# Optimization experiments

Hardware: AMD Instinct MI355X
Metric: run time of the kernel (lower is better)

The kernel has to match this reference:

```python
import jax, jax.numpy as jnp
import numpy as np

SEQ, LABEL, PRED = 96, 48, 96
DEC_LEN = LABEL + PRED  # 144
D_MODEL, N_HEADS, D_FF, C, NF = 512, 8, 2048, 7, 4
E = D_MODEL // N_HEADS  # 64
M_ENC = min(64, SEQ // 2)      # 48 modes, encoder self-attn
M_DEC = min(64, DEC_LEN // 2)  # 64 modes, decoder self / cross-q
M_KV = min(64, SEQ // 2)       # 48 modes, cross-kv
KMA = 25                       # moving-average kernel
E_LAYERS = 2
B = 128


def series_decomp(x):
    # moving average with edge replication padding (matches torch AvgPool1d version)
    p = (KMA - 1) // 2
    xp = jnp.concatenate([jnp.repeat(x[:, :1], p, axis=1), x, jnp.repeat(x[:, -1:], p, axis=1)], axis=1)
    cs = jnp.cumsum(xp, axis=1)
    cs = jnp.concatenate([jnp.zeros_like(cs[:, :1]), cs], axis=1)
    mean = (cs[:, KMA:] - cs[:, :-KMA]) / KMA  # [B,L,C]
    return x - mean, mean


def circ_conv(x, w):
    # Conv1d kernel=3, padding=1, padding_mode='circular', no bias. x [B,L,Cin], w [Cout,Cin,3]
    xp = jnp.concatenate([x[:, -1:], x, x[:, :1]], axis=1)
    return (jnp.einsum('blc,oc->blo', xp[:, :-2], w[:, :, 0])
            + jnp.einsum('blc,oc->blo', xp[:, 1:-1], w[:, :, 1])
            + jnp.einsum('blc,oc->blo', xp[:, 2:], w[:, :, 2]))


def my_layernorm(x, w, b):
    mu = jnp.mean(x, axis=-1, keepdims=True)
    var = jnp.mean((x - mu) ** 2, axis=-1, keepdims=True)
    xh = (x - mu) / jnp.sqrt(var + 1e-5) * w + b
    return xh - jnp.mean(xh, axis=1, keepdims=True)  # subtract per-batch time mean


def embed(x, mark, conv_w, time_w):
    # DataEmbedding_wo_pos: circular token conv + timeF linear (both bias-free)
    return circ_conv(x, conv_w) + mark @ time_w.T


def cplx(w):
    return jax.lax.complex(w[..., 0], w[..., 1])


def fourier_block(q, w, L):
    # q [B,L,H,E]; w complex [H,E,E,M]; low-frequency mode select -> first M rfft bins
    x = jnp.transpose(q, (0, 2, 3, 1))      # [B,H,E,L]
    x_ft = jnp.fft.rfft(x, axis=-1)
    M = w.shape[-1]
    out_sel = jnp.einsum('bhem,heom->bhom', x_ft[..., :M], w)
    out_ft = jnp.zeros_like(x_ft).at[..., :M].set(out_sel)
    return jnp.fft.irfft(out_ft, n=L, axis=-1)  # [B,H,E,L]


def fourier_cross(q, k, w, Lq):
    # FourierCrossAttention, activation='tanh' (complex tanh); v unused as in original
    xq_ft = jnp.fft.rfft(jnp.transpose(q, (0, 2, 3, 1)), axis=-1)[..., :M_DEC]
    xk_ft = jnp.fft.rfft(jnp.transpose(k, (0, 2, 3, 1)), axis=-1)[..., :M_KV]
    xqk = jnp.tanh(jnp.einsum('bhex,bhey->bhxy', xq_ft, xk_ft))
    xqkv = jnp.einsum('bhxy,bhey->bhex', xqk, xk_ft)
    xqkvw = jnp.einsum('bhex,heox->bhox', xqkv, w)
    out_ft = jnp.zeros(xqkvw.shape[:-1] + (Lq // 2 + 1,), dtype=xqkvw.dtype)
    out_ft = out_ft.at[..., :M_DEC].set(xqkvw)
    return jnp.fft.irfft(out_ft / (D_MODEL * D_MODEL), n=Lq, axis=-1)  # [B,H,E,Lq]


def attn_layer(inner, q_in, k_in, v_in, qw, qb, kw, kb, vw, vb, ow, ob):
    Bb, L, _ = q_in.shape
    S = k_in.shape[1]
    q = (q_in @ qw.T + qb).reshape(Bb, L, N_HEADS, E)
    k = (k_in @ kw.T + kb).reshape(Bb, S, N_HEADS, E)
    v = (v_in @ vw.T + vb).reshape(Bb, S, N_HEADS, E)
    out = inner(q, k, v)                   # [B,H,E,L]
    out = out.reshape(Bb, L, N_HEADS * E)  # row-major reinterpret, matches torch .view quirk
    return out @ ow.T + ob


def _forward(x_enc, x_mark_enc, x_dec, x_mark_dec,
             enc_emb_conv_w, enc_emb_time_w, dec_emb_conv_w, dec_emb_time_w,
             enc_qw, enc_qb, enc_kw, enc_kb, enc_vw, enc_vb, enc_ow, enc_ob,
             enc_fw, enc_c1, enc_c2, enc_norm_w, enc_norm_b,
             ds_qw, ds_qb, ds_kw, ds_kb, ds_vw, ds_vb, ds_ow, ds_ob, ds_fw,
             dc_qw, dc_qb, dc_kw, dc_kb, dc_vw, dc_vb, dc_ow, dc_ob, dc_fw,
             dec_c1, dec_c2, dec_trend_w, dec_norm_w, dec_norm_b, proj_w, proj_b):
    Bb = x_enc.shape[0]
    mean = jnp.broadcast_to(jnp.mean(x_enc, axis=1, keepdims=True), (Bb, PRED, C))
    seasonal_init, trend_init = series_decomp(x_enc)
    seasonal_init = jnp.pad(seasonal_init[:, -LABEL:, :], ((0, 0), (0, PRED), (0, 0)))
    trend_init = jnp.concatenate([trend_init[:, -LABEL:, :], mean], axis=1)

    # encoder
    x = embed(x_enc, x_mark_enc, enc_emb_conv_w, enc_emb_time_w)
    for l in range(E_LAYERS):
        fw = cplx(enc_fw[l])
        new_x = attn_layer(lambda q, k, v: fourier_block(q, fw, SEQ),
                           x, x, x, enc_qw[l], enc_qb[l], enc_kw[l], enc_kb[l],
                           enc_vw[l], enc_vb[l], enc_ow[l], enc_ob[l])
        x, _ = series_decomp(x + new_x)
        y = jax.nn.gelu(jnp.einsum('bld,fd->blf', x, enc_c1[l]), approximate=False)
        y = jnp.einsum('blf,df->bld', y, enc_c2[l])
        x, _ = series_decomp(x + y)
    enc_out = my_layernorm(x, enc_norm_w, enc_norm_b)

    # decoder (single layer)
    x = embed(seasonal_init, x_mark_dec, dec_emb_conv_w, dec_emb_time_w)
    fw_s = cplx(ds_fw)
    fw_c = cplx(dc_fw)
    x = x + attn_layer(lambda q, k, v: fourier_block(q, fw_s, DEC_LEN),
                       x, x, x, ds_qw, ds_qb, ds_kw, ds_kb, ds_vw, ds_vb, ds_ow, ds_ob)
    x, t1 = series_decomp(x)
    x = x + attn_layer(lambda q, k, v: fourier_cross(q, k, fw_c, DEC_LEN),
                       x, enc_out, enc_out, dc_qw, dc_qb, dc_kw, dc_kb, dc_vw, dc_vb, dc_ow, dc_ob)
    x, t2 = series_decomp(x)
    y = jax.nn.gelu(jnp.einsum('bld,fd->blf', x, dec_c1), approximate=False)
    y = jnp.einsum('blf,df->bld', y, dec_c2)
    x, t3 = series_decomp(x + y)
    residual_trend = circ_conv(t1 + t2 + t3, dec_trend_w)  # [B,144,C]
    trend = trend_init + residual_trend
    x = my_layernorm(x, dec_norm_w, dec_norm_b)
    seasonal = x @ proj_w.T + proj_b
    return (trend + seasonal)[:, -PRED:, :]


def setup_inputs() -> dict:
    keys = iter(jax.random.split(jax.random.key(0), 64))

    def n(shape, s=0.02):
        return jax.random.normal(next(keys), shape, dtype=jnp.float32) * s

    def u(shape):
        # torch.rand cfloat scaled by 1/(in_ch*out_ch), stored as trailing (re,im) pair
        return jax.random.uniform(next(keys), shape, dtype=jnp.float32) / (D_MODEL * D_MODEL)

    return dict(
        x_enc=jax.random.normal(next(keys), (B, SEQ, C), dtype=jnp.float32),
        x_mark_enc=jax.random.normal(next(keys), (B, SEQ, NF), dtype=jnp.float32),
        x_dec=jax.random.normal(next(keys), (B, DEC_LEN, C), dtype=jnp.float32),
        x_mark_dec=jax.random.normal(next(keys), (B, DEC_LEN, NF), dtype=jnp.float32),
        enc_emb_conv_w=n((D_MODEL, C, 3)),
        enc_emb_time_w=n((D_MODEL, NF)),
        dec_emb_conv_w=n((D_MODEL, C, 3)),
        dec_emb_time_w=n((D_MODEL, NF)),
        enc_qw=n((E_LAYERS, D_MODEL, D_MODEL)), enc_qb=n((E_LAYERS, D_MODEL)),
        enc_kw=n((E_LAYERS, D_MODEL, D_MODEL)), enc_kb=n((E_LAYERS, D_MODEL)),
        enc_vw=n((E_LAYERS, D_MODEL, D_MODEL)), enc_vb=n((E_LAYERS, D_MODEL)),
        enc_ow=n((E_LAYERS, D_MODEL, D_MODEL)), enc_ob=n((E_LAYERS, D_MODEL)),
        enc_fw=u((E_LAYERS, N_HEADS, E, E, M_ENC, 2)),
        enc_c1=n((E_LAYERS, D_FF, D_MODEL)), enc_c2=n((E_LAYERS, D_MODEL, D_FF)),
        enc_norm_w=jnp.ones((D_MODEL,), jnp.float32), enc_norm_b=jnp.zeros((D_MODEL,), jnp.float32),
        ds_qw=n((D_MODEL, D_MODEL)), ds_qb=n((D_MODEL,)),
        ds_kw=n((D_MODEL, D_MODEL)), ds_kb=n((D_MODEL,)),
        ds_vw=n((D_MODEL, D_MODEL)), ds_vb=n((D_MODEL,)),
        ds_ow=n((D_MODEL, D_MODEL)), ds_ob=n((D_MODEL,)),
        ds_fw=u((N_HEADS, E, E, M_DEC, 2)),
        dc_qw=n((D_MODEL, D_MODEL)), dc_qb=n((D_MODEL,)),
        dc_kw=n((D_MODEL, D_MODEL)), dc_kb=n((D_MODEL,)),
        dc_vw=n((D_MODEL, D_MODEL)), dc_vb=n((D_MODEL,)),
        dc_ow=n((D_MODEL, D_MODEL)), dc_ob=n((D_MODEL,)),
        dc_fw=u((N_HEADS, E, E, M_DEC, 2)),
        dec_c1=n((D_FF, D_MODEL)), dec_c2=n((D_MODEL, D_FF)),
        dec_trend_w=n((C, D_MODEL, 3)),
        dec_norm_w=jnp.ones((D_MODEL,), jnp.float32), dec_norm_b=jnp.zeros((D_MODEL,), jnp.float32),
        proj_w=n((C, D_MODEL)), proj_b=jnp.zeros((C,), jnp.float32),
    )


def reference(x_enc, x_mark_enc, x_dec, x_mark_dec,
              enc_emb_conv_w, enc_emb_time_w, dec_emb_conv_w, dec_emb_time_w,
              enc_qw, enc_qb, enc_kw, enc_kb, enc_vw, enc_vb, enc_ow, enc_ob,
              enc_fw, enc_c1, enc_c2, enc_norm_w, enc_norm_b,
              ds_qw, ds_qb, ds_kw, ds_kb, ds_vw, ds_vb, ds_ow, ds_ob, ds_fw,
              dc_qw, dc_qb, dc_kw, dc_kb, dc_vw, dc_vb, dc_ow, dc_ob, dc_fw,
              dec_c1, dec_c2, dec_trend_w, dec_norm_w, dec_norm_b, proj_w, proj_b):
    return _forward(x_enc, x_mark_enc, x_dec, x_mark_dec,
                    enc_emb_conv_w, enc_emb_time_w, dec_emb_conv_w, dec_emb_time_w,
                    enc_qw, enc_qb, enc_kw, enc_kb, enc_vw, enc_vb, enc_ow, enc_ob,
                    enc_fw, enc_c1, enc_c2, enc_norm_w, enc_norm_b,
                    ds_qw, ds_qb, ds_kw, ds_kb, ds_vw, ds_vb, ds_ow, ds_ob, ds_fw,
                    dc_qw, dc_qb, dc_kw, dc_kb, dc_vw, dc_vb, dc_ow, dc_ob, dc_fw,
                    dec_c1, dec_c2, dec_trend_w, dec_norm_w, dec_norm_b, proj_w, proj_b)
```

## Files before the change

kernel.cpp:

```cpp
#include <hip/hip_runtime.h>
#include <hip/hip_bf16.h>
#include <math.h>


#define PI_F 3.14159265358979323846f

typedef short bf16x8 __attribute__((ext_vector_type(8)));
typedef float f32x4 __attribute__((ext_vector_type(4)));

static __device__ __forceinline__ int iclamp(int v, int lo, int hi) {
    return v < lo ? lo : (v > hi ? hi : v);
}
static __device__ __forceinline__ unsigned pack2(float x, float y) {
    unsigned xu = __float_as_uint(x) + 0x8000u;
    unsigned yu = __float_as_uint(y) + 0x8000u;
    return (xu >> 16) | (yu & 0xFFFF0000u);
}
static __device__ __forceinline__ unsigned short bfr(float x) {
    return (unsigned short)((__float_as_uint(x) + 0x8000u) >> 16);
}
static __device__ __forceinline__ float bf2f(unsigned short s) {
    return __uint_as_float((unsigned)s << 16);
}

__global__ void zero_out_kernel(float* __restrict__ out, int n) {
    int i = blockIdx.x * 256 + threadIdx.x;
    if (i < n) out[i] = 0.f;
}

struct F2BArgs {
    const float* s[11];
    unsigned short* d[11];
    int boff[12];
};
__global__ void f2b_multi(F2BArgs a) {
    int blk = blockIdx.x;
    int seg = 0;
    while (blk >= a.boff[seg + 1]) seg++;
    int i = (blk - a.boff[seg]) * 1024 + threadIdx.x * 4;
    const float4 v = *(const float4*)(a.s[seg] + i);
    *(uint2*)(a.d[seg] + i) = make_uint2(pack2(v.x, v.y), pack2(v.z, v.w));
}

__global__ void preprocess_kernel(const float* __restrict__ xe,
                                  float* __restrict__ SI, float* __restrict__ TI) {
    int idx = blockIdx.x * 256 + threadIdx.x;
    if (idx >= 128 * 144 * 7) return;
    int c = idx % 7;
    int l = (idx / 7) % 144;
    int b = idx / (7 * 144);
    const float* xb = xe + (size_t)b * 96 * 7;
    if (l < 48) {
        int p = 48 + l;
        float sum = 0.f;
        for (int j = -12; j <= 12; j++) sum += xb[iclamp(p + j, 0, 95) * 7 + c];
        float ma = sum * (1.0f / 25.0f);
        SI[idx] = xb[p * 7 + c] - ma;
        TI[idx] = ma;
    } else {
        SI[idx] = 0.f;
        float m = 0.f;
        for (int l2 = 0; l2 < 96; l2++) m += xb[l2 * 7 + c];
        TI[idx] = m * (1.0f / 96.0f);
    }
}

__global__ void embed_feat(const float* __restrict__ x, const float* __restrict__ mark,
                           unsigned short* __restrict__ F, int L) {
    int row = blockIdx.x * 256 + threadIdx.x;
    if (row >= 128 * L) return;
    int l = row % L;
    int b = row / L;
    int lm = (l == 0) ? L - 1 : l - 1;
    int lp = (l == L - 1) ? 0 : l + 1;
    const float* x0 = x + (size_t)b * L * 7;
    const float* mk = mark + (size_t)row * 4;
    union { unsigned short s[64]; uint4 u[8]; } f;
#pragma unroll
    for (int k = 0; k < 8; k++) f.u[k] = make_uint4(0u, 0u, 0u, 0u);
#pragma unroll
    for (int c = 0; c < 7; c++) {
        f.s[c * 3 + 0] = bfr(x0[lm * 7 + c]);
        f.s[c * 3 + 1] = bfr(x0[l * 7 + c]);
        f.s[c * 3 + 2] = bfr(x0[lp * 7 + c]);
    }
#pragma unroll
    for (int j = 0; j < 4; j++) f.s[21 + j] = bfr(mk[j]);
    uint4* dst = (uint4*)(F + (size_t)row * 64);
#pragma unroll
    for (int k = 0; k < 8; k++) dst[k] = f.u[k];
}

__global__ void embed_wpack(const float* __restrict__ cw, const float* __restrict__ tw,
                            unsigned short* __restrict__ Wc) {
    int o = blockIdx.x * 256 + threadIdx.x;
    if (o >= 512) return;
    union { unsigned short s[64]; uint4 u[8]; } f;
#pragma unroll
    for (int k = 0; k < 8; k++) f.u[k] = make_uint4(0u, 0u, 0u, 0u);
#pragma unroll
    for (int c = 0; c < 7; c++) {
        const float* w = cw + (o * 7 + c) * 3;
        f.s[c * 3 + 0] = bfr(w[0]);
        f.s[c * 3 + 1] = bfr(w[1]);
        f.s[c * 3 + 2] = bfr(w[2]);
    }
#pragma unroll
    for (int j = 0; j < 4; j++) f.s[21 + j] = bfr(tw[o * 4 + j]);
    uint4* dst = (uint4*)(Wc + (size_t)o * 64);
#pragma unroll
    for (int k = 0; k < 8; k++) dst[k] = f.u[k];
}

__global__ __launch_bounds__(256, 2) void gemm_bb(
    const unsigned short* __restrict__ A, const unsigned short* __restrict__ W,
    const float* __restrict__ bias, float* __restrict__ Cf,
    unsigned short* __restrict__ Cb,
    int N, int K, int lda, int ldw, int gelu, int accum) {
    __shared__ unsigned short As[2][128 * 64];
    __shared__ unsigned short Ws[2][128 * 64];
    const int tid = threadIdx.x;
    const int lane = tid & 63, wv = tid >> 6;
    const int wm = (wv & 1) * 64, wn = (wv >> 1) * 64;
    const int q = lane >> 4, ln = lane & 15;
    const size_t bm = (size_t)blockIdx.y * 128;
    const size_t bn = (size_t)blockIdx.x * 128;

    f32x4 acc[4][4];
#pragma unroll
    for (int i = 0; i < 4; i++)
#pragma unroll
        for (int j = 0; j < 4; j++) acc[i][j] = (f32x4){0.f, 0.f, 0.f, 0.f};

    const int nt = K >> 6;

    auto stage = [&](int kt, int buf) {
        const int k0 = kt << 6;
#pragma unroll
        for (int t = 0; t < 4; t++) {
            int idx = (wv * 4 + t) * 64 + lane;
            int row = idx >> 3, cp = idx & 7;
            int cl = cp ^ (row & 7);
            __builtin_amdgcn_global_load_lds(
                (const __attribute__((address_space(1))) void*)(A + (bm + row) * lda + k0 + cl * 8),
                (__attribute__((address_space(3))) void*)(&As[buf][(size_t)(wv * 4 + t) * 512]),
                16, 0, 0);
            __builtin_amdgcn_global_load_lds(
                (const __attribute__((address_space(1))) void*)(W + (bn + row) * ldw + k0 + cl * 8),
                (__attribute__((address_space(3))) void*)(&Ws[buf][(size_t)(wv * 4 + t) * 512]),
                16, 0, 0);
        }
    };

    auto compute = [&](int buf) {
#pragma unroll
        for (int kk = 0; kk < 64; kk += 32) {
            bf16x8 af[4], bw[4];
            const int cq = (kk >> 3) + q;
#pragma unroll
            for (int i = 0; i < 4; i++) {
                int r = wm + i * 16 + ln;
                af[i] = *(const bf16x8*)(&As[buf][r * 64 + ((cq ^ (r & 7)) * 8)]);
                int rw = wn + i * 16 + ln;
                bw[i] = *(const bf16x8*)(&Ws[buf][rw * 64 + ((cq ^ (rw & 7)) * 8)]);
            }
#pragma unroll
            for (int i = 0; i < 4; i++)
#pragma unroll
                for (int j = 0; j < 4; j++)
                    acc[i][j] = __builtin_amdgcn_mfma_f32_16x16x32_bf16(
                        af[i], bw[j], acc[i][j], 0, 0, 0);
        }
    };

    stage(0, 0);
    if (nt > 1) stage(1, 1);
    for (int t = 0; t < nt - 1; t++) {
        asm volatile("s_waitcnt vmcnt(8)" ::: "memory");
        __builtin_amdgcn_s_barrier();
        compute(t & 1);
        __builtin_amdgcn_s_barrier();
        if (t + 2 < nt) stage(t + 2, t & 1);
    }
    asm volatile("s_waitcnt vmcnt(0)" ::: "memory");
    __builtin_amdgcn_s_barrier();
    compute((nt - 1) & 1);

#pragma unroll
    for (int j = 0; j < 4; j++) {
        int col = (int)bn + wn + j * 16 + ln;
        float bv = bias ? bias[col] : 0.f;
#pragma unroll
        for (int i = 0; i < 4; i++) {
            size_t row0 = bm + wm + i * 16 + q * 4;
#pragma unroll
            for (int r = 0; r < 4; r++) {
                float v = acc[i][j][r] + bv;
                if (gelu) v = 0.5f * v * (1.f + erff(v * 0.70710678118654752f));
                if (Cf) {
                    float* p = Cf + (row0 + r) * N + col;
                    if (accum) v += *p;
                    *p = v;
                }
                if (Cb) Cb[(row0 + r) * N + col] = bfr(v);
            }
        }
    }
}

__global__ void dtab_kernel(unsigned short* __restrict__ T, int M, int L, int ldk) {
    int i = blockIdx.x * 256 + threadIdx.x;
    if (i >= 128 * ldk) return;
    int n = i / ldk, k = i - n * ldk;
    float val = 0.f;
    if (n < 2 * M && k < L) {
        int m = n >> 1;
        int r = (m * k) % L;
        float ang = -2.f * PI_F * (float)r / (float)L;
        val = (n & 1) ? sinf(ang) : cosf(ang);
    }
    T[i] = bfr(val);
}
__global__ void itab_kernel(unsigned short* __restrict__ T, int M, int L, int K) {
    int i = blockIdx.x * 256 + threadIdx.x;
    if (i >= L * K) return;
    int n = i / K, k = i - n * K;
    int m = k >> 1;
    float c = (m == 0) ? 1.f : 2.f;
    int r = (m * n) % L;
    float ang = 2.f * PI_F * (float)r / (float)L;
    float val = (k & 1) ? -c * sinf(ang) : c * cosf(ang);
    T[i] = bfr(val);
}

__global__ __launch_bounds__(256) void dft_mfma2(
    const unsigned short* __restrict__ P, const unsigned short* __restrict__ Tdb,
    unsigned short* __restrict__ XT, int L, int ldk, int M) {
    __shared__ unsigned short tile[128 * 130];
    const int tid = threadIdx.x;
    const int lane = tid & 63, wv = tid >> 6;
    const int wm = (wv & 1) * 64, wn = (wv >> 1) * 64;
    const int q = lane >> 4, ln = lane & 15;
    const int bm = blockIdx.y;
    const int b = bm >> 2, c0 = (bm & 3) * 128;
    const int h0 = c0 >> 6;
    const unsigned short* Pb = P + (size_t)b * L * 512;

    f32x4 acc[4][4];
#pragma unroll
    for (int i = 0; i < 4; i++)
#pragma unroll
        for (int j = 0; j < 4; j++) acc[i][j] = (f32x4){0.f, 0.f, 0.f, 0.f};

    for (int k0 = 0; k0 < L; k0 += 32) {
        bf16x8 af[4], bf[4];
        union FR { bf16x8 v; unsigned short s[8]; };
#pragma unroll
        for (int i = 0; i < 4; i++) {
            int c = c0 + wm + i * 16 + ln;
            FR fr;
#pragma unroll
            for (int t = 0; t < 8; t++) {
                int l = k0 + q * 8 + t;
                fr.s[t] = (l < L) ? Pb[(size_t)l * 512 + c] : (unsigned short)0;
            }
            af[i] = fr.v;
        }
#pragma unroll
        for (int j = 0; j < 4; j++) {
            int n = wn + j * 16 + ln;
            bf[j] = *(const bf16x8*)(Tdb + (size_t)n * ldk + k0 + q * 8);
        }
#pragma unroll
        for (int i = 0; i < 4; i++)
#pragma unroll
            for (int j = 0; j < 4; j++)
                acc[i][j] = __builtin_amdgcn_mfma_f32_16x16x32_bf16(
                    af[i], bf[j], acc[i][j], 0, 0, 0);
    }
#pragma unroll
    for (int j = 0; j < 4; j++) {
        int col = wn + j * 16 + ln;
#pragma unroll
        for (int i = 0; i < 4; i++) {
            int r0 = wm + i * 16 + q * 4;
#pragma unroll
            for (int r = 0; r < 4; r++)
                tile[(r0 + r) * 130 + col] = bfr(acc[i][j][r]);
        }
    }
    __syncthreads();
    unsigned* XTu = (unsigned*)XT;
    for (int idx = tid; idx < 2 * M * 64; idx += 256) {
        int chunk = idx >> 6, e = idx & 63;
        int h2 = chunk / M, m = chunk - h2 * M;
        unsigned v = *(const unsigned*)&tile[(h2 * 64 + e) * 130 + 2 * m];
        XTu[((size_t)((h0 + h2) * M + m) * 128 + b) * 64 + e] = v;
    }
}

__global__ __launch_bounds__(256) void wtrans3(
    const float* __restrict__ w, unsigned short* __restrict__ WB, int M) {
    __shared__ float Lre[16 * 289], Lim[16 * 289];
    const int h = blockIdx.y;
    const int ot = blockIdx.x >> 1, et = blockIdx.x & 1;
    const int o0 = ot * 8, e0 = et * 32;
    const int tid = threadIdx.x;
    unsigned* WBu = (unsigned*)WB;
    for (int mc = 0; mc < M; mc += 16) {
        for (int idx = tid; idx < 4096; idx += 256) {
            int e = idx >> 7, o = (idx >> 4) & 7, mm = idx & 15;
            const float2 v = *(const float2*)(
                w + ((((size_t)h * 64 + e0 + e) * 64 + o0 + o) * M + mc + mm) * 2);
            Lre[mm * 289 + e * 9 + o] = v.x;
            Lim[mm * 289 + e * 9 + o] = v.y;
        }
        __syncthreads();
        for (int widx = tid; widx < 8192; widx += 256) {
            int mm = widx >> 9, no = (widx >> 5) & 15, e = widx & 31;
            int ol = no >> 1, qn = no & 1;
            float re = Lre[mm * 289 + e * 9 + ol];
            float im = Lim[mm * 289 + e * 9 + ol];
            unsigned v = qn ? pack2(im, re) : pack2(re, -im);
            WBu[((size_t)(h * M + mc + mm) * 128 + 2 * (o0 + ol) + qn) * 64 + e0 + e] = v;
        }
        __syncthreads();
    }
}

__global__ __launch_bounds__(256) void mix_v2(
    const unsigned short* __restrict__ XT, const unsigned short* __restrict__ WB,
    unsigned short* __restrict__ Yp, int M) {
    __shared__ unsigned short tile[128 * 130];
    const int m = blockIdx.x, h = blockIdx.y;
    const int tid = threadIdx.x;
    const int lane = tid & 63, wv = tid >> 6;
    const int wm = (wv & 1) * 64, wn = (wv >> 1) * 64;
    const int q = lane >> 4, ln = lane & 15;
    const size_t hm = (size_t)h * M + m;
    const unsigned short* Ab = XT + hm * 16384;
    const unsigned short* Bb = WB + hm * 16384;

    f32x4 acc[4][4];
#pragma unroll
    for (int i = 0; i < 4; i++)
#pragma unroll
        for (int j = 0; j < 4; j++) acc[i][j] = (f32x4){0.f, 0.f, 0.f, 0.f};

#pragma unroll
    for (int k0 = 0; k0 < 128; k0 += 32) {
        bf16x8 af[4], bf[4];
#pragma unroll
        for (int i = 0; i < 4; i++)
            af[i] = *(const bf16x8*)(Ab + (size_t)(wm + i * 16 + ln) * 128 + k0 + q * 8);
#pragma unroll
        for (int j = 0; j < 4; j++)
            bf[j] = *(const bf16x8*)(Bb + (size_t)(wn + j * 16 + ln) * 128 + k0 + q * 8);
#pragma unroll
        for (int i = 0; i < 4; i++)
#pragma unroll
            for (int j = 0; j < 4; j++)
                acc[i][j] = __builtin_amdgcn_mfma_f32_16x16x32_bf16(
                    af[i], bf[j], acc[i][j], 0, 0, 0);
    }
#pragma unroll
    for (int j = 0; j < 4; j++) {
        int col = wn + j * 16 + ln;
#pragma unroll
        for (int i = 0; i < 4; i++) {
            int r0 = wm + i * 16 + q * 4;
#pragma unroll
            for (int r = 0; r < 4; r++)
                tile[(r0 + r) * 130 + col] = bfr(acc[i][j][r]);
        }
    }
    __syncthreads();
    unsigned* Yu = (unsigned*)Yp;
    for (int idx = tid; idx < 128 * 64; idx += 256) {
        int b = idx >> 6, dw = idx & 63;
        unsigned v = *(const unsigned*)&tile[b * 130 + 2 * dw];
        Yu[(hm * 128 + b) * 64 + dw] = v;
    }
}

__global__ __launch_bounds__(256) void idft_v2(
    const unsigned short* __restrict__ Yp, const unsigned short* __restrict__ Tib,
    unsigned short* __restrict__ Out, int L, int K, int M, float s) {
    __shared__ unsigned short sh[2 * 64 * 132];
    const int tid = threadIdx.x;
    const int lane = tid & 63, wv = tid >> 6;
    const int wm = (wv & 1) * 64, wn = (wv >> 1) * 64;
    const int q = lane >> 4, ln = lane & 15;
    const int bm = blockIdx.y;
    const int b = bm >> 2, h0 = (bm & 3) * 2;
    const int bn = blockIdx.x * 128;

    const unsigned* Yu = (const unsigned*)Yp;
    for (int idx = tid; idx < 2 * M * 64; idx += 256) {
        int chunk = idx >> 6, dw = idx & 63;
        int h2 = chunk / M, m = chunk - h2 * M;
        unsigned v = Yu[((size_t)((h0 + h2) * M + m) * 128 + b) * 64 + dw];
        *(unsigned*)&sh[chunk * 132 + 2 * dw] = v;
    }
    __syncthreads();

    f32x4 acc[4][4];
#pragma unroll
    for (int i = 0; i < 4; i++)
#pragma unroll
        for (int j = 0; j < 4; j++) acc[i][j] = (f32x4){0.f, 0.f, 0.f, 0.f};

    for (int k0 = 0; k0 < K; k0 += 32) {
        bf16x8 af[4], bf[4];
        union FR { bf16x8 v; unsigned u[4]; };
#pragma unroll
        for (int i = 0; i < 4; i++) {
            int lr = wm + i * 16 + ln;
            int h2 = lr >> 6, o = lr & 63;
            FR fr;
#pragma unroll
            for (int jj = 0; jj < 4; jj++) {
                int m = (k0 >> 1) + q * 4 + jj;
                fr.u[jj] = *(const unsigned*)&sh[(h2 * M + m) * 132 + 2 * o];
            }
            af[i] = fr.v;
        }
#pragma unroll
        for (int j = 0; j < 4; j++) {
            int n = bn + wn + j * 16 + ln;
            if (n < L) bf[j] = *(const bf16x8*)(Tib + (size_t)n * K + k0 + q * 8);
            else bf[j] = (bf16x8){0, 0, 0, 0, 0, 0, 0, 0};
        }
#pragma unroll
        for (int i = 0; i < 4; i++)
#pragma unroll
            for (int j = 0; j < 4; j++)
                acc[i][j] = __builtin_amdgcn_mfma_f32_16x16x32_bf16(
                    af[i], bf[j], acc[i][j], 0, 0, 0);
    }
#pragma unroll
    for (int j = 0; j < 4; j++) {
        int col = bn + wn + j * 16 + ln;
        if (col >= L) continue;
#pragma unroll
        for (int i = 0; i < 4; i++) {
            int row0 = bm * 128 + wm + i * 16 + q * 4;
#pragma unroll
            for (int r = 0; r < 4; r++)
                Out[(size_t)(row0 + r) * L + col] = bfr(acc[i][j][r] * s);
        }
    }
}

__global__ __launch_bounds__(256) void xqk3(
    const unsigned short* __restrict__ XTQ, const unsigned short* __restrict__ XTK,
    unsigned* __restrict__ G) {
    __shared__ __align__(16) unsigned char sm[43520];
    unsigned short* Qs = (unsigned short*)sm;
    unsigned short* Bs = (unsigned short*)(sm + 17408);
    float* Ss = (float*)sm;
    const int b = blockIdx.x, h = blockIdx.y;
    const int tid = threadIdx.x;
    const int lane = tid & 63, wv = tid >> 6;
    const int wm = (wv & 1) * 32, wn = (wv >> 1) * 48;
    const int q = lane >> 4, ln = lane & 15;

    const uint4* Qg = (const uint4*)XTQ;
    for (int i = tid; i < 64 * 16; i += 256) {
        int x = i >> 4, c = i & 15;
        *(uint4*)(Qs + x * 136 + c * 8) = Qg[((size_t)(h * 64 + x) * 128 + b) * 16 + c];
    }
    const unsigned* Ku = (const unsigned*)XTK;
    unsigned* Bu = (unsigned*)Bs;
    for (int i = tid; i < 48 * 64; i += 256) {
        int y = i >> 6, e = i & 63;
        unsigned v = Ku[((size_t)(h * 48 + y) * 128 + b) * 64 + e];
        Bu[y * 68 + e] = v ^ 0x80000000u;
        Bu[(48 + y) * 68 + e] = (v >> 16) | (v << 16);
    }
    __syncthreads();

    f32x4 acc[2][3];
#pragma unroll
    for (int i = 0; i < 2; i++)
#pragma unroll
        for (int j = 0; j < 3; j++) acc[i][j] = (f32x4){0.f, 0.f, 0.f, 0.f};

#pragma unroll
    for (int k0 = 0; k0 < 128; k0 += 32) {
        bf16x8 af[2], bf[3];
#pragma unroll
        for (int i = 0; i < 2; i++)
            af[i] = *(const bf16x8*)(Qs + (wm + i * 16 + ln) * 136 + k0 + q * 8);
#pragma unroll
        for (int j = 0; j < 3; j++)
            bf[j] = *(const bf16x8*)(Bs + (wn + j * 16 + ln) * 136 + k0 + q * 8);
#pragma unroll
        for (int i = 0; i < 2; i++)
#pragma unroll
            for (int j = 0; j < 3; j++)
                acc[i][j] = __builtin_amdgcn_mfma_f32_16x16x32_bf16(
                    af[i], bf[j], acc[i][j], 0, 0, 0);
    }
    __syncthreads();
#pragma unroll
    for (int j = 0; j < 3; j++) {
        int col = wn + j * 16 + ln;
#pragma unroll
        for (int i = 0; i < 2; i++) {
            int r0 = wm + i * 16 + q * 4;
#pragma unroll
            for (int r = 0; r < 4; r++)
                Ss[(r0 + r) * 100 + col] = acc[i][j][r];
        }
    }
    __syncthreads();
    for (int i = tid; i < 3072; i += 256) {
        int x = i / 48, y = i - x * 48;
        float re = Ss[x * 100 + y], im = Ss[x * 100 + 48 + y];
        float a2 = 2.f * re, b2 = 2.f * im;
        a2 = fminf(fmaxf(a2, -80.f), 80.f);
        float denom = coshf(a2) + cosf(b2);
        G[((size_t)(b * 8 + h) * 64 + x) * 48 + y] =
            pack2(sinhf(a2) / denom, sinf(b2) / denom);
    }
}

__global__ __launch_bounds__(256) void xqkv3(
    const unsigned* __restrict__ G, const unsigned short* __restrict__ XTK,
    unsigned short* __restrict__ VT) {
    __shared__ __align__(16) unsigned char sm[26624];
    unsigned short* Bs = (unsigned short*)sm;
    unsigned short* Vs = (unsigned short*)sm;
    const int b = blockIdx.x, h = blockIdx.y;
    const int tid = threadIdx.x;
    const int lane = tid & 63, wv = tid >> 6;
    const int wm = (wv & 1) * 32, wn = (wv >> 1) * 64;
    const int q = lane >> 4, ln = lane & 15;

    const unsigned* Ku = (const unsigned*)XTK;
    unsigned* Bu = (unsigned*)Bs;
    for (int i = tid; i < 48 * 64; i += 256) {
        int y = i >> 6, e = i & 63;
        unsigned v = Ku[((size_t)(h * 48 + y) * 128 + b) * 64 + e];
        Bu[(2 * e) * 52 + y] = v ^ 0x80000000u;
        Bu[(2 * e + 1) * 52 + y] = (v >> 16) | (v << 16);
    }
    __syncthreads();

    const unsigned short* Ag = (const unsigned short*)G + (size_t)(b * 8 + h) * 6144;
    f32x4 acc[2][4];
#pragma unroll
    for (int i = 0; i < 2; i++)
#pragma unroll
        for (int j = 0; j < 4; j++) acc[i][j] = (f32x4){0.f, 0.f, 0.f, 0.f};

#pragma unroll
    for (int k0 = 0; k0 < 96; k0 += 32) {
        bf16x8 af[2], bf[4];
#pragma unroll
        for (int i = 0; i < 2; i++)
            af[i] = *(const bf16x8*)(Ag + (wm + i * 16 + ln) * 96 + k0 + q * 8);
#pragma unroll
        for (int j = 0; j < 4; j++)
            bf[j] = *(const bf16x8*)(Bs + (wn + j * 16 + ln) * 104 + k0 + q * 8);
#pragma unroll
        for (int i = 0; i < 2; i++)
#pragma unroll
            for (int j = 0; j < 4; j++)
                acc[i][j] = __builtin_amdgcn_mfma_f32_16x16x32_bf16(
                    af[i], bf[j], acc[i][j], 0, 0, 0);
    }
    __syncthreads();
#pragma unroll
    for (int j = 0; j < 4; j++) {
        int col = wn + j * 16 + ln;
#pragma unroll
        for (int i = 0; i < 2; i++) {
            int r0 = wm + i * 16 + q * 4;
#pragma unroll
            for (int r = 0; r < 4; r++)
                Vs[(r0 + r) * 132 + col] = bfr(acc[i][j][r]);
        }
    }
    __syncthreads();
    unsigned* Vu = (unsigned*)VT;
    for (int i = tid; i < 64 * 64; i += 256) {
        int x = i >> 6, dw = i & 63;
        Vu[((size_t)(h * 64 + x) * 128 + b) * 64 + dw] = *(unsigned*)&Vs[x * 132 + 2 * dw];
    }
}

__global__ void decomp_kernel(const float* __restrict__ P, const float* __restrict__ Q,
                              float* __restrict__ SO, unsigned short* __restrict__ SOb,
                              float* __restrict__ TS, int L, int tmode) {
    int b = blockIdx.x, d0 = blockIdx.y * 64;
    __shared__ float s[144 * 64];
    for (int i = threadIdx.x; i < L * 64; i += 256) {
        int l = i >> 6, d = i & 63;
        size_t idx = ((size_t)b * L + l) * 512 + d0 + d;
        float v = P[idx];
        if (Q) v += Q[idx];
        s[i] = v;
    }
    __syncthreads();
    for (int i = threadIdx.x; i < L * 64; i += 256) {
        int l = i >> 6, d = i & 63;
        float sum = 0.f;
#pragma unroll
        for (int j = -12; j <= 12; j++) sum += s[iclamp(l + j, 0, L - 1) * 64 + d];
        float ma = sum * (1.0f / 25.0f);
        size_t idx = ((size_t)b * L + l) * 512 + d0 + d;
        float so = s[i] - ma;
        SO[idx] = so;
        if (SOb) SOb[idx] = bfr(so);
        if (tmode == 1) TS[idx] = ma;
        else if (tmode == 2) TS[idx] += ma;
    }
}

__global__ __launch_bounds__(256) void ln_rows_kernel(const float* __restrict__ in,
                                                      const float* __restrict__ w,
                                                      const float* __restrict__ bvec,
                                                      float* __restrict__ out) {
    size_t row = blockIdx.x;
    const float* p = in + row * 512;
    int t = threadIdx.x;
    float v0 = p[t], v1 = p[t + 256];
    float s = v0 + v1, s2 = v0 * v0 + v1 * v1;
    for (int o = 32; o > 0; o >>= 1) {
        s += __shfl_xor(s, o, 64);
        s2 += __shfl_xor(s2, o, 64);
    }
    __shared__ float rs[4], rs2[4];
    int wid = t >> 6;
    if ((t & 63) == 0) { rs[wid] = s; rs2[wid] = s2; }
    __syncthreads();
    s = rs[0] + rs[1] + rs[2] + rs[3];
    s2 = rs2[0] + rs2[1] + rs2[2] + rs2[3];
    float mu = s * (1.0f / 512.0f);
    float var = s2 * (1.0f / 512.0f) - mu * mu;
    float r = rsqrtf(var + 1e-5f);
    out[row * 512 + t] = (v0 - mu) * r * w[t] + bvec[t];
    out[row * 512 + t + 256] = (v1 - mu) * r * w[t + 256] + bvec[t + 256];
}

__global__ void timesub_kernel(float* __restrict__ X, unsigned short* __restrict__ Xb,
                               int L) {
    int b = blockIdx.x, d0 = blockIdx.y * 64;
    __shared__ float tile[144 * 64];
    __shared__ float mean[64];
    for (int i = threadIdx.x; i < L * 64; i += 256) {
        int l = i >> 6, d = i & 63;
        tile[i] = X[((size_t)b * L + l) * 512 + d0 + d];
    }
    __syncthreads();
    if (threadIdx.x < 64) {
        float sm = 0.f;
        for (int l = 0; l < L; l++) sm += tile[l * 64 + threadIdx.x];
        mean[threadIdx.x] = sm / (float)L;
    }
    __syncthreads();
    for (int i = threadIdx.x; i < L * 64; i += 256) {
        int l = i >> 6, d = i & 63;
        size_t idx = ((size_t)b * L + l) * 512 + d0 + d;
        float v = tile[i] - mean[d];
        X[idx] = v;
        if (Xb) Xb[idx] = bfr(v);
    }
}

__global__ __launch_bounds__(256) void final_v2(
    const float* __restrict__ XL, const float* __restrict__ TS,
    const float* __restrict__ TI, const float* __restrict__ trend_w,
    const float* __restrict__ proj_w, const float* __restrict__ proj_b,
    float* __restrict__ out) {
    int blk = blockIdx.x;
    int b = blk / 96, lo = blk - b * 96;
    int l = lo + 48;
    int lm = l - 1;
    int lp = (l == 143) ? 0 : l + 1;
    const float* ts = TS + (size_t)b * 144 * 512;
    const float* r0 = ts + (size_t)lm * 512;
    const float* r1 = ts + (size_t)l * 512;
    const float* r2 = ts + (size_t)lp * 512;
    const float* xl = XL + ((size_t)b * 144 + l) * 512;
    int t = threadIdx.x;
    float p[7];
#pragma unroll
    for (int c = 0; c < 7; c++) p[c] = 0.f;
#pragma unroll
    for (int dd = 0; dd < 2; dd++) {
        int d = t + dd * 256;
        float a0 = r0[d], a1 = r1[d], a2 = r2[d], x = xl[d];
#pragma unroll
        for (int c = 0; c < 7; c++) {
            const float* tw = trend_w + ((size_t)c * 512 + d) * 3;
            float v = a0 * tw[0] + a1 * tw[1] + a2 * tw[2];
            v = fmaf(x, proj_w[c * 512 + d], v);
            p[c] += v;
        }
    }
#pragma unroll
    for (int o = 32; o > 0; o >>= 1)
#pragma unroll
        for (int c = 0; c < 7; c++) p[c] += __shfl_xor(p[c], o, 64);
    __shared__ float red[4][7];
    int wid = t >> 6;
    if ((t & 63) == 0)
#pragma unroll
        for (int c = 0; c < 7; c++) red[wid][c] = p[c];
    __syncthreads();
    if (t < 7) {
        float v = red[0][t] + red[1][t] + red[2][t] + red[3][t]
                + TI[((size_t)b * 144 + l) * 7 + t] + proj_b[t];
        out[(size_t)blk * 7 + t] = v;
    }
}

static inline int cdiv(int a, int b) { return (a + b - 1) / b; }

extern "C" void kernel_launch(void* const* d_in, const int* in_sizes, int n_in,
                              void* d_out, int out_size, void* d_ws, size_t ws_size,
                              hipStream_t stream) {
    const float* x_enc      = (const float*)d_in[0];
    const float* x_mark_enc = (const float*)d_in[1];
    const float* x_mark_dec = (const float*)d_in[3];
    const float* enc_emb_conv_w = (const float*)d_in[4];
    const float* enc_emb_time_w = (const float*)d_in[5];
    const float* dec_emb_conv_w = (const float*)d_in[6];
    const float* dec_emb_time_w = (const float*)d_in[7];
    const float* enc_qw = (const float*)d_in[8];
    const float* enc_qb = (const float*)d_in[9];
    const float* enc_ow = (const float*)d_in[14];
    const float* enc_ob = (const float*)d_in[15];
    const float* enc_fw = (const float*)d_in[16];
    const float* enc_c1 = (const float*)d_in[17];
    const float* enc_c2 = (const float*)d_in[18];
    const float* enc_norm_w = (const float*)d_in[19];
    const float* enc_norm_b = (const float*)d_in[20];
    const float* ds_qw = (const float*)d_in[21];
    const float* ds_qb = (const float*)d_in[22];
    const float* ds_ow = (const float*)d_in[27];
    const float* ds_ob = (const float*)d_in[28];
    const float* ds_fw = (const float*)d_in[29];
    const float* dc_qw = (const float*)d_in[30];
    const float* dc_qb = (const float*)d_in[31];
    const float* dc_kw = (const float*)d_in[32];
    const float* dc_kb = (const float*)d_in[33];
    const float* dc_ow = (const float*)d_in[36];
    const float* dc_ob = (const float*)d_in[37];
    const float* dc_fw = (const float*)d_in[38];
    const float* dec_c1 = (const float*)d_in[39];
    const float* dec_c2 = (const float*)d_in[40];
    const float* dec_trend_w = (const float*)d_in[41];
    const float* dec_norm_w = (const float*)d_in[42];
    const float* dec_norm_b = (const float*)d_in[43];
    const float* proj_w = (const float*)d_in[44];
    const float* proj_b = (const float*)d_in[45];

    float* ws = (float*)d_ws;
    float* XD   = ws;
    float* TS   = ws + 9437184;
    float* XE   = ws + 18874368;
    unsigned short* XEb = (unsigned short*)(ws + 25165824);
    unsigned short* XDb = (unsigned short*)(ws + 28311552);
    float* SI   = ws + 33030144;
    float* TI   = ws + 33159168;
    float* TAB  = ws + 33288192;
    unsigned short* WF = (unsigned short*)(ws + 33320960);
    float* SC   = ws + 37646336;
    unsigned short* TdbE = (unsigned short*)(TAB);
    unsigned short* TdbD = (unsigned short*)(TAB + 6144);
    unsigned short* TibE = (unsigned short*)(TAB + 16384);
    unsigned short* TibD = (unsigned short*)(TAB + 20992);
    unsigned short* Fb  = (unsigned short*)(ws + 51277824);
    unsigned short* Wcb = (unsigned short*)(ws + 51867648);

    unsigned short* enc_qw_b = WF;
    unsigned short* enc_ow_b = WF + 524288;
    unsigned short* enc_c1_b = WF + 1048576;
    unsigned short* enc_c2_b = WF + 3145728;
    unsigned short* ds_qw_b  = WF + 5242880;
    unsigned short* ds_ow_b  = WF + 5505024;
    unsigned short* dc_qw_b  = WF + 5767168;
    unsigned short* dc_kw_b  = WF + 6029312;
    unsigned short* dc_ow_b  = WF + 6291456;
    unsigned short* dec_c1_b = WF + 6553600;
    unsigned short* dec_c2_b = WF + 7602176;

    const size_t need_bytes = (size_t)53768192 * sizeof(float);
    if (ws_size < need_bytes) {
        zero_out_kernel<<<cdiv(out_size, 256), 256, 0, stream>>>((float*)d_out, out_size);
        return;
    }

    auto gemm = [&](const unsigned short* A, const unsigned short* W, const float* bias,
                    float* Cf, unsigned short* Cb, int rows, int N, int K,
                    int lda, int ldw, int gelu, int accum) {
        dim3 g(N / 128, rows / 128);
        gemm_bb<<<g, 256, 0, stream>>>(A, W, bias, Cf, Cb, N, K, lda, ldw, gelu, accum);
    };

    {
        F2BArgs fa;
        const float* srcs[11] = {enc_qw, enc_ow, enc_c1, enc_c2, ds_qw, ds_ow,
                                 dc_qw, dc_kw, dc_ow, dec_c1, dec_c2};
        unsigned short* dsts[11] = {enc_qw_b, enc_ow_b, enc_c1_b, enc_c2_b, ds_qw_b,
                                    ds_ow_b, dc_qw_b, dc_kw_b, dc_ow_b, dec_c1_b, dec_c2_b};
        const int ns[11] = {524288, 524288, 2097152, 2097152, 262144, 262144,
                            262144, 262144, 262144, 1048576, 1048576};
        int off = 0;
        fa.boff[0] = 0;
        for (int i = 0; i < 11; i++) {
            fa.s[i] = srcs[i];
            fa.d[i] = dsts[i];
            off += ns[i] / 1024;
            fa.boff[i + 1] = off;
        }
        f2b_multi<<<off, 256, 0, stream>>>(fa);
    }

    dtab_kernel<<<cdiv(128 * 96, 256), 256, 0, stream>>>(TdbE, 48, 96, 96);
    dtab_kernel<<<cdiv(128 * 160, 256), 256, 0, stream>>>(TdbD, 64, 144, 160);
    itab_kernel<<<cdiv(96 * 96, 256), 256, 0, stream>>>(TibE, 48, 96, 96);
    itab_kernel<<<cdiv(144 * 128, 256), 256, 0, stream>>>(TibD, 64, 144, 128);

    preprocess_kernel<<<cdiv(128 * 144 * 7, 256), 256, 0, stream>>>(x_enc, SI, TI);
    embed_wpack<<<2, 256, 0, stream>>>(enc_emb_conv_w, enc_emb_time_w, Wcb);
    embed_feat<<<48, 256, 0, stream>>>(x_enc, x_mark_enc, Fb, 96);
    gemm(Fb, Wcb, nullptr, XE, XEb, 12288, 512, 64, 64, 64, 0, 0);

    for (int l = 0; l < 2; l++) {
        const unsigned short* qwb = enc_qw_b + (size_t)l * 262144;
        const float* qb = enc_qb + (size_t)l * 512;
        const unsigned short* owb = enc_ow_b + (size_t)l * 262144;
        const float* ob = enc_ob + (size_t)l * 512;
        const float* fw = enc_fw + (size_t)l * 8 * 64 * 64 * 48 * 2;
        const unsigned short* c1b = enc_c1_b + (size_t)l * 1048576;
        const unsigned short* c2b = enc_c2_b + (size_t)l * 1048576;
        unsigned short* Pq = (unsigned short*)(SC);
        unsigned short* XT = (unsigned short*)(SC + 3145728);
        unsigned short* WB = (unsigned short*)(SC + 6291456);
        unsigned short* Yp = (unsigned short*)(SC + 9437184);
        unsigned short* Tidb = (unsigned short*)(SC);
        float* To = SC + 3145728;

        gemm(XEb, qwb, qb, nullptr, Pq, 12288, 512, 512, 512, 512, 0, 0);
        dft_mfma2<<<dim3(1, 512), 256, 0, stream>>>(Pq, TdbE, XT, 96, 96, 48);
        wtrans3<<<dim3(16, 8), 256, 0, stream>>>(fw, WB, 48);
        mix_v2<<<dim3(48, 8), 256, 0, stream>>>(XT, WB, Yp, 48);
        idft_v2<<<dim3(1, 512), 256, 0, stream>>>(Yp, TibE, Tidb, 96, 96, 48, 1.f / 96.f);
        gemm(Tidb, owb, ob, To, nullptr, 12288, 512, 512, 512, 512, 0, 0);
        decomp_kernel<<<dim3(128, 8), 256, 0, stream>>>(XE, To, XE, XEb, nullptr, 96, 0);
        unsigned short* hid = (unsigned short*)(SC);
        gemm(XEb, c1b, nullptr, nullptr, hid, 12288, 2048, 512, 512, 512, 1, 0);
        gemm(hid, c2b, nullptr, TS, nullptr, 12288, 512, 2048, 2048, 2048, 0, 0);
        decomp_kernel<<<dim3(128, 8), 256, 0, stream>>>(XE, TS, XE, XEb, nullptr, 96, 0);
    }
    ln_rows_kernel<<<12288, 256, 0, stream>>>(XE, enc_norm_w, enc_norm_b, XE);
    timesub_kernel<<<dim3(128, 8), 256, 0, stream>>>(XE, XEb, 96);

    embed_wpack<<<2, 256, 0, stream>>>(dec_emb_conv_w, dec_emb_time_w, Wcb);
    embed_feat<<<72, 256, 0, stream>>>(SI, x_mark_dec, Fb, 144);
    gemm(Fb, Wcb, nullptr, XD, XDb, 18432, 512, 64, 64, 64, 0, 0);

    {
        unsigned short* Pq = (unsigned short*)(SC);
        unsigned short* XT = (unsigned short*)(SC + 4718592);
        unsigned short* WB = (unsigned short*)(SC + 8912896);
        unsigned short* Yp = (unsigned short*)(SC);
        unsigned short* Tidb = (unsigned short*)(SC + 9437184);
        float* To = SC;

        gemm(XDb, ds_qw_b, ds_qb, nullptr, Pq, 18432, 512, 512, 512, 512, 0, 0);
        dft_mfma2<<<dim3(1, 512), 256, 0, stream>>>(Pq, TdbD, XT, 144, 160, 64);
        wtrans3<<<dim3(16, 8), 256, 0, stream>>>(ds_fw, WB, 64);
        mix_v2<<<dim3(64, 8), 256, 0, stream>>>(XT, WB, Yp, 64);
        idft_v2<<<dim3(2, 512), 256, 0, stream>>>(Yp, TibD, Tidb, 144, 128, 64, 1.f / 144.f);
        gemm(Tidb, ds_ow_b, ds_ob, To, nullptr, 18432, 512, 512, 512, 512, 0, 0);
        decomp_kernel<<<dim3(128, 8), 256, 0, stream>>>(XD, To, XD, XDb, TS, 144, 1);
    }

    {
        unsigned short* Pq  = (unsigned short*)(SC);
        unsigned short* XTQ = (unsigned short*)(SC + 4718592);
        unsigned short* Pk  = (unsigned short*)(SC);
        unsigned short* XTK = (unsigned short*)(SC + 8912896);
        unsigned* G         = (unsigned*)(SC);
        unsigned short* VT  = (unsigned short*)(SC + 3145728);
        unsigned short* WB  = (unsigned short*)(SC + 7340032);
        unsigned short* Yp  = (unsigned short*)(SC + 11534336);
        unsigned short* Tidb = (unsigned short*)(SC);
        float* To = SC + 4718592;

        gemm(XDb, dc_qw_b, dc_qb, nullptr, Pq, 18432, 512, 512, 512, 512, 0, 0);
        dft_mfma2<<<dim3(1, 512), 256, 0, stream>>>(Pq, TdbD, XTQ, 144, 160, 64);
        gemm(XEb, dc_kw_b, dc_kb, nullptr, Pk, 12288, 512, 512, 512, 512, 0, 0);
        dft_mfma2<<<dim3(1, 512), 256, 0, stream>>>(Pk, TdbE, XTK, 96, 96, 48);
        xqk3<<<dim3(128, 8), 256, 0, stream>>>(XTQ, XTK, G);
        xqkv3<<<dim3(128, 8), 256, 0, stream>>>(G, XTK, VT);
        wtrans3<<<dim3(16, 8), 256, 0, stream>>>(dc_fw, WB, 64);
        mix_v2<<<dim3(64, 8), 256, 0, stream>>>(VT, WB, Yp, 64);
        idft_v2<<<dim3(2, 512), 256, 0, stream>>>(Yp, TibD, Tidb, 144, 128, 64,
                                                  1.f / (144.f * 262144.f));
        gemm(Tidb, dc_ow_b, dc_ob, To, nullptr, 18432, 512, 512, 512, 512, 0, 0);
        decomp_kernel<<<dim3(128, 8), 256, 0, stream>>>(XD, To, XD, XDb, TS, 144, 2);
    }

    {
        unsigned short* hid = (unsigned short*)(SC);
        float* fout = XE;
        for (int j0 = 0; j0 < 2048; j0 += 1024) {
            gemm(XDb, dec_c1_b + (size_t)j0 * 512, nullptr, nullptr, hid,
                 18432, 1024, 512, 512, 512, 1, 0);
            gemm(hid, dec_c2_b + j0, nullptr, fout, nullptr,
                 18432, 512, 1024, 1024, 2048, 0, j0 > 0);
        }
        decomp_kernel<<<dim3(128, 8), 256, 0, stream>>>(XD, fout, XD, nullptr, TS, 144, 2);
    }

    ln_rows_kernel<<<18432, 256, 0, stream>>>(XD, dec_norm_w, dec_norm_b, XD);
    timesub_kernel<<<dim3(128, 8), 256, 0, stream>>>(XD, nullptr, 144);
    final_v2<<<12288, 256, 0, stream>>>(
        XD, TS, TI, dec_trend_w, proj_w, proj_b, (float*)d_out);
}
```

Before: 1.535 ms.

## Emit transposed Q projections for DFT, add XCD-aware GEMM remap and unpipelined variant

```diff
diff --git a/kernel.cpp b/kernel.cpp
--- a/kernel.cpp
+++ b/kernel.cpp
@@ -112,19 +112,27 @@
     for (int k = 0; k < 8; k++) dst[k] = f.u[k];
 }
 
-__global__ __launch_bounds__(256, 2) void gemm_bb(
+template <int PIPE>
+__global__ __launch_bounds__(256, PIPE ? 2 : 4) void gemm_bb(
     const unsigned short* __restrict__ A, const unsigned short* __restrict__ W,
     const float* __restrict__ bias, float* __restrict__ Cf,
     unsigned short* __restrict__ Cb,
-    int N, int K, int lda, int ldw, int gelu, int accum) {
-    __shared__ unsigned short As[2][128 * 64];
-    __shared__ unsigned short Ws[2][128 * 64];
+    int N, int K, int lda, int ldw, int gelu, int accum, int brow) {
+    __shared__ unsigned short As[(PIPE ? 2 : 1)][128 * 64];
+    __shared__ unsigned short Ws[(PIPE ? 2 : 1)][128 * 64];
     const int tid = threadIdx.x;
     const int lane = tid & 63, wv = tid >> 6;
     const int wm = (wv & 1) * 64, wn = (wv >> 1) * 64;
     const int q = lane >> 4, ln = lane & 15;
-    const size_t bm = (size_t)blockIdx.y * 128;
-    const size_t bn = (size_t)blockIdx.x * 128;
+
+    const int nbx = gridDim.x;
+    const int nwg = nbx * gridDim.y;
+    const int orig = blockIdx.y * nbx + blockIdx.x;
+    const int qq = nwg >> 3, rr = nwg & 7;
+    const int xcd = orig & 7, lid = orig >> 3;
+    const int wgid = (xcd < rr ? xcd * (qq + 1) : rr * (qq + 1) + (xcd - rr) * qq) + lid;
+    const size_t bm = (size_t)(wgid / nbx) * 128;
+    const size_t bn = (size_t)(wgid % nbx) * 128;
 
     f32x4 acc[4][4];
 #pragma unroll
@@ -173,29 +181,39 @@
         }
     };
 
-    stage(0, 0);
-    if (nt > 1) stage(1, 1);
-    for (int t = 0; t < nt - 1; t++) {
-        asm volatile("s_waitcnt vmcnt(8)" ::: "memory");
+    if (PIPE) {
+        stage(0, 0);
+        if (nt > 1) stage(1, 1);
+        for (int t = 0; t < nt - 1; t++) {
+            asm volatile("s_waitcnt vmcnt(8)" ::: "memory");
+            __builtin_amdgcn_s_barrier();
+            compute(t & 1);
+            __builtin_amdgcn_s_barrier();
+            if (t + 2 < nt) stage(t + 2, t & 1);
+        }
+        asm volatile("s_waitcnt vmcnt(0)" ::: "memory");
         __builtin_amdgcn_s_barrier();
-        compute(t & 1);
-        __builtin_amdgcn_s_barrier();
-        if (t + 2 < nt) stage(t + 2, t & 1);
-    }
-    asm volatile("s_waitcnt vmcnt(0)" ::: "memory");
-    __builtin_amdgcn_s_barrier();
-    compute((nt - 1) & 1);
+        compute((nt - 1) & 1);
+    } else {
+        for (int t = 0; t < nt; t++) {
+            stage(t, 0);
+            __syncthreads();
+            compute(0);
+            __syncthreads();
+        }
+    }
 
 #pragma unroll
     for (int j = 0; j < 4; j++) {
         int col = (int)bn + wn + j * 16 + ln;
-        float bv = bias ? bias[col] : 0.f;
+        float bv = (bias && !brow) ? bias[col] : 0.f;
 #pragma unroll
         for (int i = 0; i < 4; i++) {
             size_t row0 = bm + wm + i * 16 + q * 4;
 #pragma unroll
             for (int r = 0; r < 4; r++) {
                 float v = acc[i][j][r] + bv;
+                if (brow && bias) v += bias[row0 + r];
                 if (gelu) v = 0.5f * v * (1.f + erff(v * 0.70710678118654752f));
                 if (Cf) {
                     float* p = Cf + (row0 + r) * N + col;
@@ -234,8 +252,8 @@
 }
 
 __global__ __launch_bounds__(256) void dft_mfma2(
-    const unsigned short* __restrict__ P, const unsigned short* __restrict__ Tdb,
-    unsigned short* __restrict__ XT, int L, int ldk, int M) {
+    const unsigned short* __restrict__ PT, const unsigned short* __restrict__ Tdb,
+    unsigned short* __restrict__ XT, int L, int ldk, int M, int Mtot) {
     __shared__ unsigned short tile[128 * 130];
     const int tid = threadIdx.x;
     const int lane = tid & 63, wv = tid >> 6;
@@ -244,7 +262,6 @@
     const int bm = blockIdx.y;
     const int b = bm >> 2, c0 = (bm & 3) * 128;
     const int h0 = c0 >> 6;
-    const unsigned short* Pb = P + (size_t)b * L * 512;
 
     f32x4 acc[4][4];
 #pragma unroll
@@ -254,17 +271,13 @@
 
     for (int k0 = 0; k0 < L; k0 += 32) {
         bf16x8 af[4], bf[4];
-        union FR { bf16x8 v; unsigned short s[8]; };
+        const bool ok = (k0 + q * 8 < L);
+        const size_t base = (size_t)b * L + k0 + q * 8;
 #pragma unroll
         for (int i = 0; i < 4; i++) {
             int c = c0 + wm + i * 16 + ln;
-            FR fr;
-#pragma unroll
-            for (int t = 0; t < 8; t++) {
-                int l = k0 + q * 8 + t;
-                fr.s[t] = (l < L) ? Pb[(size_t)l * 512 + c] : (unsigned short)0;
-            }
-            af[i] = fr.v;
+            af[i] = ok ? *(const bf16x8*)(PT + (size_t)c * Mtot + base)
+                       : (bf16x8){0, 0, 0, 0, 0, 0, 0, 0};
         }
 #pragma unroll
         for (int j = 0; j < 4; j++) {
@@ -797,9 +810,14 @@
 
     auto gemm = [&](const unsigned short* A, const unsigned short* W, const float* bias,
                     float* Cf, unsigned short* Cb, int rows, int N, int K,
-                    int lda, int ldw, int gelu, int accum) {
+                    int lda, int ldw, int gelu, int accum, int pipe, int brow) {
         dim3 g(N / 128, rows / 128);
-        gemm_bb<<<g, 256, 0, stream>>>(A, W, bias, Cf, Cb, N, K, lda, ldw, gelu, accum);
+        if (pipe)
+            gemm_bb<1><<<g, 256, 0, stream>>>(A, W, bias, Cf, Cb, N, K, lda, ldw,
+                                              gelu, accum, brow);
+        else
+            gemm_bb<0><<<g, 256, 0, stream>>>(A, W, bias, Cf, Cb, N, K, lda, ldw,
+                                              gelu, accum, brow);
     };
 
     {
@@ -829,7 +847,7 @@
     preprocess_kernel<<<cdiv(128 * 144 * 7, 256), 256, 0, stream>>>(x_enc, SI, TI);
     embed_wpack<<<2, 256, 0, stream>>>(enc_emb_conv_w, enc_emb_time_w, Wcb);
     embed_feat<<<48, 256, 0, stream>>>(x_enc, x_mark_enc, Fb, 96);
-    gemm(Fb, Wcb, nullptr, XE, XEb, 12288, 512, 64, 64, 64, 0, 0);
+    gemm(Fb, Wcb, nullptr, XE, XEb, 12288, 512, 64, 64, 64, 0, 0, 0, 0);
 
     for (int l = 0; l < 2; l++) {
         const unsigned short* qwb = enc_qw_b + (size_t)l * 262144;
@@ -839,23 +857,23 @@
         const float* fw = enc_fw + (size_t)l * 8 * 64 * 64 * 48 * 2;
         const unsigned short* c1b = enc_c1_b + (size_t)l * 1048576;
         const unsigned short* c2b = enc_c2_b + (size_t)l * 1048576;
-        unsigned short* Pq = (unsigned short*)(SC);
+        unsigned short* PT = (unsigned short*)(SC);
         unsigned short* XT = (unsigned short*)(SC + 3145728);
         unsigned short* WB = (unsigned short*)(SC + 6291456);
         unsigned short* Yp = (unsigned short*)(SC + 9437184);
         unsigned short* Tidb = (unsigned short*)(SC);
         float* To = SC + 3145728;
 
-        gemm(XEb, qwb, qb, nullptr, Pq, 12288, 512, 512, 512, 512, 0, 0);
-        dft_mfma2<<<dim3(1, 512), 256, 0, stream>>>(Pq, TdbE, XT, 96, 96, 48);
+        gemm(qwb, XEb, qb, nullptr, PT, 512, 12288, 512, 512, 512, 0, 0, 0, 1);
+        dft_mfma2<<<dim3(1, 512), 256, 0, stream>>>(PT, TdbE, XT, 96, 96, 48, 12288);
         wtrans3<<<dim3(16, 8), 256, 0, stream>>>(fw, WB, 48);
         mix_v2<<<dim3(48, 8), 256, 0, stream>>>(XT, WB, Yp, 48);
         idft_v2<<<dim3(1, 512), 256, 0, stream>>>(Yp, TibE, Tidb, 96, 96, 48, 1.f / 96.f);
-        gemm(Tidb, owb, ob, To, nullptr, 12288, 512, 512, 512, 512, 0, 0);
+        gemm(Tidb, owb, ob, To, nullptr, 12288, 512, 512, 512, 512, 0, 0, 0, 0);
         decomp_kernel<<<dim3(128, 8), 256, 0, stream>>>(XE, To, XE, XEb, nullptr, 96, 0);
         unsigned short* hid = (unsigned short*)(SC);
-        gemm(XEb, c1b, nullptr, nullptr, hid, 12288, 2048, 512, 512, 512, 1, 0);
-        gemm(hid, c2b, nullptr, TS, nullptr, 12288, 512, 2048, 2048, 2048, 0, 0);
+        gemm(XEb, c1b, nullptr, nullptr, hid, 12288, 2048, 512, 512, 512, 1, 0, 1, 0);
+        gemm(hid, c2b, nullptr, TS, nullptr, 12288, 512, 2048, 2048, 2048, 0, 0, 1, 0);
         decomp_kernel<<<dim3(128, 8), 256, 0, stream>>>(XE, TS, XE, XEb, nullptr, 96, 0);
     }
     ln_rows_kernel<<<12288, 256, 0, stream>>>(XE, enc_norm_w, enc_norm_b, XE);
@@ -863,29 +881,29 @@
 
     embed_wpack<<<2, 256, 0, stream>>>(dec_emb_conv_w, dec_emb_time_w, Wcb);
     embed_feat<<<72, 256, 0, stream>>>(SI, x_mark_dec, Fb, 144);
-    gemm(Fb, Wcb, nullptr, XD, XDb, 18432, 512, 64, 64, 64, 0, 0);
+    gemm(Fb, Wcb, nullptr, XD, XDb, 18432, 512, 64, 64, 64, 0, 0, 0, 0);
 
     {
-        unsigned short* Pq = (unsigned short*)(SC);
+        unsigned short* PT = (unsigned short*)(SC);
         unsigned short* XT = (unsigned short*)(SC + 4718592);
         unsigned short* WB = (unsigned short*)(SC + 8912896);
         unsigned short* Yp = (unsigned short*)(SC);
         unsigned short* Tidb = (unsigned short*)(SC + 9437184);
         float* To = SC;
 
-        gemm(XDb, ds_qw_b, ds_qb, nullptr, Pq, 18432, 512, 512, 512, 512, 0, 0);
-        dft_mfma2<<<dim3(1, 512), 256, 0, stream>>>(Pq, TdbD, XT, 144, 160, 64);
+        gemm(ds_qw_b, XDb, ds_qb, nullptr, PT, 512, 18432, 512, 512, 512, 0, 0, 0, 1);
+        dft_mfma2<<<dim3(1, 512), 256, 0, stream>>>(PT, TdbD, XT, 144, 160, 64, 18432);
         wtrans3<<<dim3(16, 8), 256, 0, stream>>>(ds_fw, WB, 64);
         mix_v2<<<dim3(64, 8), 256, 0, stream>>>(XT, WB, Yp, 64);
         idft_v2<<<dim3(2, 512), 256, 0, stream>>>(Yp, TibD, Tidb, 144, 128, 64, 1.f / 144.f);
-        gemm(Tidb, ds_ow_b, ds_ob, To, nullptr, 18432, 512, 512, 512, 512, 0, 0);
+        gemm(Tidb, ds_ow_b, ds_ob, To, nullptr, 18432, 512, 512, 512, 512, 0, 0, 0, 0);
         decomp_kernel<<<dim3(128, 8), 256, 0, stream>>>(XD, To, XD, XDb, TS, 144, 1);
     }
 
     {
-        unsigned short* Pq  = (unsigned short*)(SC);
+        unsigned short* PTq = (unsigned short*)(SC);
         unsigned short* XTQ = (unsigned short*)(SC + 4718592);
-        unsigned short* Pk  = (unsigned short*)(SC);
+        unsigned short* PTk = (unsigned short*)(SC);
         unsigned short* XTK = (unsigned short*)(SC + 8912896);
         unsigned* G         = (unsigned*)(SC);
         unsigned short* VT  = (unsigned short*)(SC + 3145728);
@@ -894,17 +912,17 @@
         unsigned short* Tidb = (unsigned short*)(SC);
         float* To = SC + 4718592;
 
-        gemm(XDb, dc_qw_b, dc_qb, nullptr, Pq, 18432, 512, 512, 512, 512, 0, 0);
-        dft_mfma2<<<dim3(1, 512), 256, 0, stream>>>(Pq, TdbD, XTQ, 144, 160, 64);
-        gemm(XEb, dc_kw_b, dc_kb, nullptr, Pk, 12288, 512, 512, 512, 512, 0, 0);
-        dft_mfma2<<<dim3(1, 512), 256, 0, stream>>>(Pk, TdbE, XTK, 96, 96, 48);
+        gemm(dc_qw_b, XDb, dc_qb, nullptr, PTq, 512, 18432, 512, 512, 512, 0, 0, 0, 1);
+        dft_mfma2<<<dim3(1, 512), 256, 0, stream>>>(PTq, TdbD, XTQ, 144, 160, 64, 18432);
+        gemm(dc_kw_b, XEb, dc_kb, nullptr, PTk, 512, 12288, 512, 512, 512, 0, 0, 0, 1);
+        dft_mfma2<<<dim3(1, 512), 256, 0, stream>>>(PTk, TdbE, XTK, 96, 96, 48, 12288);
         xqk3<<<dim3(128, 8), 256, 0, stream>>>(XTQ, XTK, G);
         xqkv3<<<dim3(128, 8), 256, 0, stream>>>(G, XTK, VT);
         wtrans3<<<dim3(16, 8), 256, 0, stream>>>(dc_fw, WB, 64);
         mix_v2<<<dim3(64, 8), 256, 0, stream>>>(VT, WB, Yp, 64);
         idft_v2<<<dim3(2, 512), 256, 0, stream>>>(Yp, TibD, Tidb, 144, 128, 64,
                                                   1.f / (144.f * 262144.f));
-        gemm(Tidb, dc_ow_b, dc_ob, To, nullptr, 18432, 512, 512, 512, 512, 0, 0);
+        gemm(Tidb, dc_ow_b, dc_ob, To, nullptr, 18432, 512, 512, 512, 512, 0, 0, 0, 0);
         decomp_kernel<<<dim3(128, 8), 256, 0, stream>>>(XD, To, XD, XDb, TS, 144, 2);
     }
 
@@ -913,9 +931,9 @@
         float* fout = XE;
         for (int j0 = 0; j0 < 2048; j0 += 1024) {
             gemm(XDb, dec_c1_b + (size_t)j0 * 512, nullptr, nullptr, hid,
-                 18432, 1024, 512, 512, 512, 1, 0);
+                 18432, 1024, 512, 512, 512, 1, 0, 1, 0);
             gemm(hid, dec_c2_b + j0, nullptr, fout, nullptr,
-                 18432, 512, 1024, 1024, 2048, 0, j0 > 0);
+                 18432, 512, 1024, 1024, 2048, 0, j0 > 0, 1, 0);
         }
         decomp_kernel<<<dim3(128, 8), 256, 0, stream>>>(XD, fout, XD, nullptr, TS, 144, 2);
     }
```

Measured after the change: 1.567 ms. 2.0% more time.
